# Kernel optimization log

Measured on AMD Instinct MI355X. Metric: run time of the kernel, lower is better.

Reference implementation:

```python
import jax, jax.numpy as jnp
import numpy as np

T, B, C, H, W = 40, 256, 32, 8, 8
D = C * H * W  # 2048 flattened enc dim


def setup_inputs() -> dict:
    key = jax.random.key(0)
    k0, k1, k2 = jax.random.split(key, 3)
    x = jax.random.normal(k0, (T, B, C, H, W), dtype=jnp.float32)
    W0 = jax.random.normal(k1, (4 * C, 2 * C, 5, 5), dtype=jnp.float32) * 0.05
    b0 = jnp.zeros((4 * C,), dtype=jnp.float32)
    W1 = jax.random.normal(k2, (4 * C, 2 * C, 3, 3), dtype=jnp.float32) * 0.05
    b1 = jnp.zeros((4 * C,), dtype=jnp.float32)
    return {"x": x, "W0": W0, "b0": b0, "W1": W1, "b1": b1}


def _conv(x, w, b, pad):
    y = jax.lax.conv_general_dilated(
        x, w, window_strides=(1, 1), padding=[(pad, pad), (pad, pad)],
        dimension_numbers=("NCHW", "OIHW", "NCHW"))
    return y + b[None, :, None, None]


def _cell(inp, h, c, w, b, pad):
    # ConvLSTMCell: conv over concat(input, hidden) -> 4 gates
    g = _conv(jnp.concatenate([inp, h], axis=1), w, b, pad)
    i_g, f_g, o_g, c_g = jnp.split(g, 4, axis=1)
    c_new = jax.nn.sigmoid(f_g) * c + jax.nn.sigmoid(i_g) * jnp.tanh(c_g)
    h_new = jax.nn.sigmoid(o_g) * jnp.tanh(c_new)
    return h_new, c_new


def reference(x, W0, b0, W1, b1):
    Tn, Bn, Cn, Hn, Wn = x.shape
    Dn = Cn * Hn * Wn
    zeros = jnp.zeros((Bn, Cn, Hn, Wn), x.dtype)
    buf0 = jnp.zeros((Tn, Bn, Dn), x.dtype)  # growing prev_encs buffer, masked
    steps = jnp.arange(Tn)

    def body(carry, xt_t):
        xt, t = xt_t
        h0, c0, h1, c1, buf = carry
        h0, c0 = _cell(xt, h0, c0, W0, b0, 2)  # cell0: k=5, pad=2
        flat = h0.reshape(Bn, Dn)
        buf = buf.at[t].set(flat)
        # attention over encs[0..t] (softmax over a single entry at t=0 -> enc itself)
        dots = jnp.einsum("bd,tbd->bt", flat, buf)
        dots = jnp.where((steps <= t)[None, :], dots, -jnp.inf)
        wts = jax.nn.softmax(dots, axis=1)
        att = jnp.einsum("bt,tbd->bd", wts, buf).reshape(Bn, Cn, Hn, Wn)
        h1, c1 = _cell(att, h1, c1, W1, b1, 1)  # cell1: k=3, pad=1
        return (h0, c0, h1, c1, buf), h1

    _, ys = jax.lax.scan(body, (zeros, zeros, zeros, zeros, buf0), (x, steps))
    return ys  # [T, B, C, 8, 8]
```

## Files before the change

### kernel.cpp

```cpp
#include <hip/hip_runtime.h>

#define TT 40
#define NB 256
#define DD 2048
#define HISTL 28

typedef __bf16 bf16x8 __attribute__((ext_vector_type(8)));
typedef float f32x4 __attribute__((ext_vector_type(4)));
typedef unsigned short u16;
typedef unsigned int u32;
typedef u16 u16x8 __attribute__((ext_vector_type(8)));
typedef u16 u16x4 __attribute__((ext_vector_type(4)));

__device__ __forceinline__ u16 f2bf(float f) {
  u32 u = __builtin_bit_cast(u32, f);
  return (u16)((u + 0x7fffu + ((u >> 16) & 1u)) >> 16);
}
__device__ __forceinline__ float bf2f(u16 h) {
  return __builtin_bit_cast(float, ((u32)h) << 16);
}
__device__ __forceinline__ bf16x8 asbf(u16x8 v) { return __builtin_bit_cast(bf16x8, v); }

__device__ __forceinline__ float sigm(float x) { return 1.0f / (1.0f + __expf(-x)); }
__device__ __forceinline__ float tanh_(float x) {
  float e = __expf(-2.0f * fabsf(x));
  float t = (1.0f - e) / (1.0f + e);
  return copysignf(t, x);
}

__device__ __forceinline__ f32x4 mfma16(bf16x8 a, bf16x8 b, f32x4 c) {
  return __builtin_amdgcn_mfma_f32_16x16x32_bf16(a, b, c, 0, 0, 0);
}

__device__ __forceinline__ int imin(int a, int b) { return a < b ? a : b; }

__global__ void prep_weights(const float* __restrict__ W0, const float* __restrict__ W1,
                             u16* __restrict__ A0, u16* __restrict__ A1) {
  int tid = blockIdx.x * 256 + threadIdx.x;
  if (tid < 25600) {
    int lane = tid & 63;
    int kt = tid >> 9;
    int p = ((tid >> 6) & 7) * 16 + (lane & 15);
    int oc = (p & 3) * 32 + ((p >> 5) & 3) * 8 + ((p >> 4) & 1) * 4 + ((p >> 2) & 3);
    int kb = kt * 32 + (lane >> 4) * 8;
#pragma unroll
    for (int j = 0; j < 8; ++j) {
      int k = kb + j;
      int pos = k >> 6, ic = k & 63;
      int ky = pos / 5, kx = pos - ky * 5;
      A0[tid * 8 + j] = f2bf(W0[((oc * 64 + ic) * 5 + ky) * 5 + kx]);
    }
  } else if (tid < 25600 + 9216) {
    int t2 = tid - 25600;
    int lane = t2 & 63;
    int kt = t2 >> 9;
    int p = ((t2 >> 6) & 7) * 16 + (lane & 15);
    int oc = (p & 3) * 32 + ((p >> 5) & 3) * 8 + ((p >> 4) & 1) * 4 + ((p >> 2) & 3);
    int kb = kt * 32 + (lane >> 4) * 8;
#pragma unroll
    for (int j = 0; j < 8; ++j) {
      int k = kb + j;
      int pos = k >> 6, ic = k & 63;
      int ky = pos / 3, kx = pos - ky * 3;
      A1[t2 * 8 + j] = f2bf(W1[((oc * 64 + ic) * 3 + ky) * 3 + kx]);
    }
  }
}

template <int KK, int NKT, int SKB, int DEPTH>
__device__ __forceinline__ void conv_loop2(const u16* __restrict__ wsA, const u16* img,
                                           int wg, int lane, f32x4 acc[2][4]) {
  const int ic0v = (lane >> 4) << 3;
  const int pb0 = ((lane & 15) >> 3) * 12 + (lane & 7);
  const bf16x8* A = (const bf16x8*)wsA;
  const int aidx = 2 * wg * 64 + lane;
  bf16x8 r0[DEPTH], r1[DEPTH];
#pragma unroll
  for (int i = 0; i < DEPTH; ++i) {
    r0[i] = A[aidx + i * 512];
    r1[i] = A[aidx + i * 512 + 64];
  }
#pragma unroll
  for (int kt = 0; kt < NKT; ++kt) {
    const int slot = kt % DEPTH;
    const bf16x8 c0 = r0[slot];
    const bf16x8 c1 = r1[slot];
    if (kt + DEPTH < NKT) {
      r0[slot] = A[aidx + (kt + DEPTH) * 512];
      r1[slot] = A[aidx + (kt + DEPTH) * 512 + 64];
    }
    const int pos = kt >> 1, ih = kt & 1;
    const int ky = pos / KK, kx = pos - ky * KK;
    const int Pb = pb0 + (ky * 12 + kx + SKB);
    const int idx = Pb * 64 + ((ic0v ^ ((Pb & 7) << 3)) ^ (ih << 5));
    u16x8 b0v = *(const u16x8*)(img + idx);
    u16x8 b1v = *(const u16x8*)(img + idx + 1536);
    u16x8 b2v = *(const u16x8*)(img + idx + 3072);
    u16x8 b3v = *(const u16x8*)(img + idx + 4608);
    acc[0][0] = mfma16(c0, asbf(b0v), acc[0][0]);
    acc[1][0] = mfma16(c1, asbf(b0v), acc[1][0]);
    acc[0][1] = mfma16(c0, asbf(b1v), acc[0][1]);
    acc[1][1] = mfma16(c1, asbf(b1v), acc[1][1]);
    acc[0][2] = mfma16(c0, asbf(b2v), acc[0][2]);
    acc[1][2] = mfma16(c1, asbf(b2v), acc[1][2]);
    acc[0][3] = mfma16(c0, asbf(b3v), acc[0][3]);
    acc[1][3] = mfma16(c1, asbf(b3v), acc[1][3]);
  }
}

__global__ void __launch_bounds__(512, 1)
convlstm_main(const float* __restrict__ x, const float* __restrict__ b0g,
              const float* __restrict__ b1g, const u16* __restrict__ wsA0,
              const u16* __restrict__ wsA1, u16* __restrict__ buf,
              float* __restrict__ out) {
  alignas(16) __shared__ u16 imgA[9216];
  alignas(16) __shared__ u16 imgB[9216];
  alignas(16) __shared__ u16 hist[HISTL * DD];
  alignas(16) __shared__ u16 curr[2 * DD];
  __shared__ float sdots[64];

  const int tid = threadIdx.x;
  const int b = blockIdx.x;
  const int lane = tid & 63;
  const int w = tid >> 6;
  const bool isA = (w < 4);
  const int wg = w & 3;
  const int h = lane >> 4;
  const int l15 = lane & 15;
  const int ch0 = 8 * wg + h;

  for (int i = tid; i < 9216; i += 512) {
    imgA[i] = 0;
    imgB[i] = 0;
  }

  float cst[2][4] = {};
  float bi[2][4];
  {
    const float* bg = isA ? b0g : b1g;
#pragma unroll
    for (int mi = 0; mi < 2; ++mi)
#pragma unroll
      for (int j = 0; j < 4; ++j) bi[mi][j] = bg[j * 32 + ch0 + 4 * mi];
  }

  const int Pldx = ((lane >> 3) + 2) * 12 + (lane & 7) + 2;
  const int swx = (Pldx & 7) << 3;
  const int Pl0 = ((l15 >> 3) + 2) * 12 + (l15 & 7) + 2;
  const int swh = (Pl0 & 7) << 3;
  const int bt = tid & 255;
  const int e8 = bt * 8;
  const int chB = bt >> 3;

  __syncthreads();

  float xr[8];
  if (isA) {
    const float* xp0 = x + (size_t)b * DD;
#pragma unroll
    for (int i = 0; i < 8; ++i) {
      int c = i * 4 + wg;
      imgA[Pldx * 64 + (c ^ swx)] = f2bf(xp0[c * 64 + lane]);
    }
    const float* xp1 = x + (size_t)(NB + b) * DD;
#pragma unroll
    for (int i = 0; i < 8; ++i) xr[i] = xp1[(i * 4 + wg) * 64 + lane];
  }

  __syncthreads();

  for (int s = 0; s <= TT + 1; ++s) {
    f32x4 acc[2][4];
    f32x4 zz = {0.f, 0.f, 0.f, 0.f};
#pragma unroll
    for (int mi = 0; mi < 2; ++mi)
#pragma unroll
      for (int nt = 0; nt < 4; ++nt) acc[mi][nt] = zz;

    if (isA) {
      if (s < TT) conv_loop2<5, 50, 0, 8>(wsA0, imgA, wg, lane, acc);
    } else {
      if (s >= 2) conv_loop2<3, 18, 13, 6>(wsA1, imgB, wg, lane, acc);
      const int t1 = s - 1;
      if (t1 >= 0 && t1 < TT) {
        u16x8 fv[4];
        const u16x8* rowT = (const u16x8*)&curr[(t1 & 1) * DD];
#pragma unroll
        for (int i = 0; i < 4; ++i) fv[i] = rowT[i * 64 + lane];
        int tp = wg;
        for (; tp <= t1 && tp < HISTL; tp += 4) {
          const u16x8* rowP = (const u16x8*)&hist[tp * DD];
          u16x8 p0 = rowP[lane], p1 = rowP[64 + lane], p2 = rowP[128 + lane],
                p3 = rowP[192 + lane];
          float d0 = 0.f, d1 = 0.f, d2 = 0.f, d3 = 0.f;
#pragma unroll
          for (int j = 0; j < 8; ++j) {
            d0 += bf2f(fv[0][j]) * bf2f(p0[j]);
            d1 += bf2f(fv[1][j]) * bf2f(p1[j]);
            d2 += bf2f(fv[2][j]) * bf2f(p2[j]);
            d3 += bf2f(fv[3][j]) * bf2f(p3[j]);
          }
          float dsum = (d0 + d1) + (d2 + d3);
#pragma unroll
          for (int off = 32; off; off >>= 1) dsum += __shfl_xor(dsum, off, 64);
          if (lane == 0) sdots[tp] = dsum;
        }
        for (; tp < t1; tp += 4) {
          const u16x8* rowP = (const u16x8*)(buf + (size_t)(tp * NB + b) * DD);
          u16x8 p0 = rowP[lane], p1 = rowP[64 + lane], p2 = rowP[128 + lane],
                p3 = rowP[192 + lane];
          float d0 = 0.f, d1 = 0.f, d2 = 0.f, d3 = 0.f;
#pragma unroll
          for (int j = 0; j < 8; ++j) {
            d0 += bf2f(fv[0][j]) * bf2f(p0[j]);
            d1 += bf2f(fv[1][j]) * bf2f(p1[j]);
            d2 += bf2f(fv[2][j]) * bf2f(p2[j]);
            d3 += bf2f(fv[3][j]) * bf2f(p3[j]);
          }
          float dsum = (d0 + d1) + (d2 + d3);
#pragma unroll
          for (int off = 32; off; off >>= 1) dsum += __shfl_xor(dsum, off, 64);
          if (lane == 0) sdots[tp] = dsum;
        }
        if (tp == t1) {
          float d0 = 0.f, d1 = 0.f, d2 = 0.f, d3 = 0.f;
#pragma unroll
          for (int j = 0; j < 8; ++j) {
            d0 += bf2f(fv[0][j]) * bf2f(fv[0][j]);
            d1 += bf2f(fv[1][j]) * bf2f(fv[1][j]);
            d2 += bf2f(fv[2][j]) * bf2f(fv[2][j]);
            d3 += bf2f(fv[3][j]) * bf2f(fv[3][j]);
          }
          float dsum = (d0 + d1) + (d2 + d3);
#pragma unroll
          for (int off = 32; off; off >>= 1) dsum += __shfl_xor(dsum, off, 64);
          if (lane == 0) sdots[tp] = dsum;
        }
      }
    }
    __syncthreads();

    if (isA) {
      if (s < TT) {
        u16* bufrow = buf + (size_t)(s * NB + b) * DD;
        u16* crow = &curr[(s & 1) * DD];
#pragma unroll
        for (int mi = 0; mi < 2; ++mi) {
          const int chm = ch0 + 4 * mi;
          u16x4 hv4;
#pragma unroll
          for (int nt = 0; nt < 4; ++nt) {
            float ig = acc[mi][nt][0] + bi[mi][0];
            float fg = acc[mi][nt][1] + bi[mi][1];
            float og = acc[mi][nt][2] + bi[mi][2];
            float cg = acc[mi][nt][3] + bi[mi][3];
            float cn = sigm(fg) * cst[mi][nt] + sigm(ig) * tanh_(cg);
            float hn = sigm(og) * tanh_(cn);
            cst[mi][nt] = cn;
            u16 hv = f2bf(hn);
            hv4[nt] = hv;
            imgA[(Pl0 + 24 * nt) * 64 + ((32 + chm) ^ swh)] = hv;
          }
          const int dbase = chm * 64 + l15 * 4;
          *(u16x4*)&crow[dbase] = hv4;
          if (s < HISTL)
            *(u16x4*)&hist[s * DD + dbase] = hv4;
          else
            *(u16x4*)(bufrow + dbase) = hv4;
        }
        if (s + 1 < TT) {
#pragma unroll
          for (int i = 0; i < 8; ++i) {
            int c = i * 4 + wg;
            imgA[Pldx * 64 + (c ^ swx)] = f2bf(xr[i]);
          }
        }
        if (s + 2 < TT) {
          const float* xp = x + (size_t)((s + 2) * NB + b) * DD;
#pragma unroll
          for (int i = 0; i < 8; ++i) xr[i] = xp[(i * 4 + wg) * 64 + lane];
        }
      }
    } else {
      const int t2 = s - 2;
      if (t2 >= 0) {
        float* outrow = out + (size_t)(t2 * NB + b) * DD;
#pragma unroll
        for (int mi = 0; mi < 2; ++mi) {
          const int chm = ch0 + 4 * mi;
#pragma unroll
          for (int nt = 0; nt < 4; ++nt) {
            float ig = acc[mi][nt][0] + bi[mi][0];
            float fg = acc[mi][nt][1] + bi[mi][1];
            float og = acc[mi][nt][2] + bi[mi][2];
            float cg = acc[mi][nt][3] + bi[mi][3];
            float cn = sigm(fg) * cst[mi][nt] + sigm(ig) * tanh_(cg);
            float hn = sigm(og) * tanh_(cn);
            cst[mi][nt] = cn;
            imgB[(Pl0 + 24 * nt) * 64 + ((32 + chm) ^ swh)] = f2bf(hn);
            outrow[chm * 64 + nt * 16 + l15] = hn;
          }
        }
      }
      const int t1 = s - 1;
      if (t1 >= 0 && t1 < TT) {
        float myw;
        {
          float v = (lane <= t1) ? sdots[lane] : -3.0e38f;
          float m = v;
#pragma unroll
          for (int off = 32; off; off >>= 1) m = fmaxf(m, __shfl_xor(m, off, 64));
          float e = (lane <= t1) ? __expf(v - m) : 0.f;
          float ss = e;
#pragma unroll
          for (int off = 32; off; off >>= 1) ss += __shfl_xor(ss, off, 64);
          myw = e / ss;
        }
        float av[8] = {0.f, 0.f, 0.f, 0.f, 0.f, 0.f, 0.f, 0.f};
        const int lim = imin(t1, HISTL);
        int tp = 0;
        for (; tp < lim; ++tp) {
          float wt = __shfl(myw, tp, 64);
          u16x8 v = *(const u16x8*)&hist[tp * DD + e8];
#pragma unroll
          for (int j = 0; j < 8; ++j) av[j] = fmaf(wt, bf2f(v[j]), av[j]);
        }
        for (tp = HISTL; tp < t1; ++tp) {
          float wt = __shfl(myw, tp, 64);
          u16x8 v = *(const u16x8*)(buf + (size_t)(tp * NB + b) * DD + e8);
#pragma unroll
          for (int j = 0; j < 8; ++j) av[j] = fmaf(wt, bf2f(v[j]), av[j]);
        }
        {
          float wt = __shfl(myw, t1, 64);
          u16x8 v = *(const u16x8*)&curr[(t1 & 1) * DD + e8];
#pragma unroll
          for (int j = 0; j < 8; ++j) av[j] = fmaf(wt, bf2f(v[j]), av[j]);
        }
#pragma unroll
        for (int j = 0; j < 8; ++j) {
          const int pixel = (j & 3) * 16 + (bt & 7) * 2 + (j >> 2);
          const int P = ((pixel >> 3) + 2) * 12 + (pixel & 7) + 2;
          imgB[P * 64 + (chB ^ ((P & 7) << 3))] = f2bf(av[j]);
        }
      }
    }
    __syncthreads();
  }
}

extern "C" void kernel_launch(void* const* d_in, const int* in_sizes, int n_in,
                              void* d_out, int out_size, void* d_ws, size_t ws_size,
                              hipStream_t stream) {
  const float* x = (const float*)d_in[0];
  const float* W0 = (const float*)d_in[1];
  const float* b0 = (const float*)d_in[2];
  const float* W1 = (const float*)d_in[3];
  const float* b1 = (const float*)d_in[4];
  float* out = (float*)d_out;

  u16* A0 = (u16*)d_ws;
  u16* A1 = A0 + 204800;
  u16* buf = (u16*)((char*)d_ws + (1 << 20));

  prep_weights<<<136, 256, 0, stream>>>(W0, W1, A0, A1);
  convlstm_main<<<256, 512, 0, stream>>>(x, b0, b1, A0, A1, buf, out);
}
```

Before: 1.313 ms.

## Double block size to 1024 threads, splitting conv M-tiles across twice the waves

Raises the workgroup from 8 to 16 waves so each wave computes one 16-row MFMA M-tile instead of two, and redistributes the attention dot products, weighted sum and x loading over the extra waves. It also swaps shuffle-based weight broadcast for readlane and unrolls the global-history loop by two. The aim is more latency hiding on this serial recurrent kernel with one block per CU. The cost is more waves per block synchronizing every step and fewer registers available per thread.

```diff
diff --git a/kernel.cpp b/kernel.cpp
--- a/kernel.cpp
+++ b/kernel.cpp
@@ -33,6 +33,10 @@
 }
 
 __device__ __forceinline__ int imin(int a, int b) { return a < b ? a : b; }
+
+__device__ __forceinline__ float rdlane(float v, int l) {
+  return __builtin_bit_cast(float, __builtin_amdgcn_readlane(__builtin_bit_cast(int, v), l));
+}
 
 __global__ void prep_weights(const float* __restrict__ W0, const float* __restrict__ W1,
                              u16* __restrict__ A0, u16* __restrict__ A1) {
@@ -68,27 +72,20 @@
 }
 
 template <int KK, int NKT, int SKB, int DEPTH>
-__device__ __forceinline__ void conv_loop2(const u16* __restrict__ wsA, const u16* img,
-                                           int wg, int lane, f32x4 acc[2][4]) {
+__device__ __forceinline__ void conv_loop1(const u16* __restrict__ wsA, const u16* img,
+                                           int wg, int lane, f32x4 acc[4]) {
   const int ic0v = (lane >> 4) << 3;
   const int pb0 = ((lane & 15) >> 3) * 12 + (lane & 7);
   const bf16x8* A = (const bf16x8*)wsA;
-  const int aidx = 2 * wg * 64 + lane;
-  bf16x8 r0[DEPTH], r1[DEPTH];
-#pragma unroll
-  for (int i = 0; i < DEPTH; ++i) {
-    r0[i] = A[aidx + i * 512];
-    r1[i] = A[aidx + i * 512 + 64];
-  }
+  const int aidx = wg * 64 + lane;
+  bf16x8 r[DEPTH];
+#pragma unroll
+  for (int i = 0; i < DEPTH; ++i) r[i] = A[aidx + i * 512];
 #pragma unroll
   for (int kt = 0; kt < NKT; ++kt) {
     const int slot = kt % DEPTH;
-    const bf16x8 c0 = r0[slot];
-    const bf16x8 c1 = r1[slot];
-    if (kt + DEPTH < NKT) {
-      r0[slot] = A[aidx + (kt + DEPTH) * 512];
-      r1[slot] = A[aidx + (kt + DEPTH) * 512 + 64];
-    }
+    const bf16x8 c0 = r[slot];
+    if (kt + DEPTH < NKT) r[slot] = A[aidx + (kt + DEPTH) * 512];
     const int pos = kt >> 1, ih = kt & 1;
     const int ky = pos / KK, kx = pos - ky * KK;
     const int Pb = pb0 + (ky * 12 + kx + SKB);
@@ -97,18 +94,14 @@
     u16x8 b1v = *(const u16x8*)(img + idx + 1536);
     u16x8 b2v = *(const u16x8*)(img + idx + 3072);
     u16x8 b3v = *(const u16x8*)(img + idx + 4608);
-    acc[0][0] = mfma16(c0, asbf(b0v), acc[0][0]);
-    acc[1][0] = mfma16(c1, asbf(b0v), acc[1][0]);
-    acc[0][1] = mfma16(c0, asbf(b1v), acc[0][1]);
-    acc[1][1] = mfma16(c1, asbf(b1v), acc[1][1]);
-    acc[0][2] = mfma16(c0, asbf(b2v), acc[0][2]);
-    acc[1][2] = mfma16(c1, asbf(b2v), acc[1][2]);
-    acc[0][3] = mfma16(c0, asbf(b3v), acc[0][3]);
-    acc[1][3] = mfma16(c1, asbf(b3v), acc[1][3]);
-  }
-}
-
-__global__ void __launch_bounds__(512, 1)
+    acc[0] = mfma16(c0, asbf(b0v), acc[0]);
+    acc[1] = mfma16(c0, asbf(b1v), acc[1]);
+    acc[2] = mfma16(c0, asbf(b2v), acc[2]);
+    acc[3] = mfma16(c0, asbf(b3v), acc[3]);
+  }
+}
+
+__global__ void __launch_bounds__(1024, 1)
 convlstm_main(const float* __restrict__ x, const float* __restrict__ b0g,
               const float* __restrict__ b1g, const u16* __restrict__ wsA0,
               const u16* __restrict__ wsA1, u16* __restrict__ buf,
@@ -123,64 +116,60 @@
   const int b = blockIdx.x;
   const int lane = tid & 63;
   const int w = tid >> 6;
-  const bool isA = (w < 4);
-  const int wg = w & 3;
+  const bool isA = (w < 8);
+  const int wg = w & 7;
   const int h = lane >> 4;
   const int l15 = lane & 15;
-  const int ch0 = 8 * wg + h;
-
-  for (int i = tid; i < 9216; i += 512) {
+  const int ch = ((wg >> 1) & 3) * 8 + (wg & 1) * 4 + h;
+
+  for (int i = tid; i < 9216; i += 1024) {
     imgA[i] = 0;
     imgB[i] = 0;
   }
 
-  float cst[2][4] = {};
-  float bi[2][4];
+  float cst[4] = {};
+  float bi[4];
   {
     const float* bg = isA ? b0g : b1g;
 #pragma unroll
-    for (int mi = 0; mi < 2; ++mi)
-#pragma unroll
-      for (int j = 0; j < 4; ++j) bi[mi][j] = bg[j * 32 + ch0 + 4 * mi];
+    for (int j = 0; j < 4; ++j) bi[j] = bg[j * 32 + ch];
   }
 
   const int Pldx = ((lane >> 3) + 2) * 12 + (lane & 7) + 2;
   const int swx = (Pldx & 7) << 3;
   const int Pl0 = ((l15 >> 3) + 2) * 12 + (l15 & 7) + 2;
   const int swh = (Pl0 & 7) << 3;
-  const int bt = tid & 255;
-  const int e8 = bt * 8;
-  const int chB = bt >> 3;
+  const int btB = tid & 511;
+  const int e4 = btB * 4;
+  const int chB = btB >> 4;
+  const int plB = btB & 15;
 
   __syncthreads();
 
-  float xr[8];
+  float xr[4];
   if (isA) {
     const float* xp0 = x + (size_t)b * DD;
-#pragma unroll
-    for (int i = 0; i < 8; ++i) {
-      int c = i * 4 + wg;
-      imgA[Pldx * 64 + (c ^ swx)] = f2bf(xp0[c * 64 + lane]);
-    }
+    u16x4 xv;
+#pragma unroll
+    for (int i = 0; i < 4; ++i) xv[i] = f2bf(xp0[(wg * 4 + i) * 64 + lane]);
+    *(u16x4*)&imgA[Pldx * 64 + ((wg * 4) ^ swx)] = xv;
     const float* xp1 = x + (size_t)(NB + b) * DD;
 #pragma unroll
-    for (int i = 0; i < 8; ++i) xr[i] = xp1[(i * 4 + wg) * 64 + lane];
+    for (int i = 0; i < 4; ++i) xr[i] = xp1[(wg * 4 + i) * 64 + lane];
   }
 
   __syncthreads();
 
   for (int s = 0; s <= TT + 1; ++s) {
-    f32x4 acc[2][4];
+    f32x4 acc[4];
     f32x4 zz = {0.f, 0.f, 0.f, 0.f};
 #pragma unroll
-    for (int mi = 0; mi < 2; ++mi)
-#pragma unroll
-      for (int nt = 0; nt < 4; ++nt) acc[mi][nt] = zz;
+    for (int nt = 0; nt < 4; ++nt) acc[nt] = zz;
 
     if (isA) {
-      if (s < TT) conv_loop2<5, 50, 0, 8>(wsA0, imgA, wg, lane, acc);
+      if (s < TT) conv_loop1<5, 50, 0, 8>(wsA0, imgA, wg, lane, acc);
     } else {
-      if (s >= 2) conv_loop2<3, 18, 13, 6>(wsA1, imgB, wg, lane, acc);
+      if (s >= 2) conv_loop1<3, 18, 13, 6>(wsA1, imgB, wg, lane, acc);
       const int t1 = s - 1;
       if (t1 >= 0 && t1 < TT) {
         u16x8 fv[4];
@@ -188,7 +177,7 @@
 #pragma unroll
         for (int i = 0; i < 4; ++i) fv[i] = rowT[i * 64 + lane];
         int tp = wg;
-        for (; tp <= t1 && tp < HISTL; tp += 4) {
+        for (; tp <= t1 && tp < HISTL; tp += 8) {
           const u16x8* rowP = (const u16x8*)&hist[tp * DD];
           u16x8 p0 = rowP[lane], p1 = rowP[64 + lane], p2 = rowP[128 + lane],
                 p3 = rowP[192 + lane];
@@ -205,7 +194,7 @@
           for (int off = 32; off; off >>= 1) dsum += __shfl_xor(dsum, off, 64);
           if (lane == 0) sdots[tp] = dsum;
         }
-        for (; tp < t1; tp += 4) {
+        for (; tp < t1; tp += 8) {
           const u16x8* rowP = (const u16x8*)(buf + (size_t)(tp * NB + b) * DD);
           u16x8 p0 = rowP[lane], p1 = rowP[64 + lane], p2 = rowP[128 + lane],
                 p3 = rowP[192 + lane];
@@ -222,7 +211,7 @@
           for (int off = 32; off; off >>= 1) dsum += __shfl_xor(dsum, off, 64);
           if (lane == 0) sdots[tp] = dsum;
         }
-        if (tp == t1) {
+        if (t1 >= HISTL && (t1 & 7) == wg) {
           float d0 = 0.f, d1 = 0.f, d2 = 0.f, d3 = 0.f;
 #pragma unroll
           for (int j = 0; j < 8; ++j) {
@@ -234,7 +223,7 @@
           float dsum = (d0 + d1) + (d2 + d3);
 #pragma unroll
           for (int off = 32; off; off >>= 1) dsum += __shfl_xor(dsum, off, 64);
-          if (lane == 0) sdots[tp] = dsum;
+          if (lane == 0) sdots[t1] = dsum;
         }
       }
     }
@@ -244,41 +233,36 @@
       if (s < TT) {
         u16* bufrow = buf + (size_t)(s * NB + b) * DD;
         u16* crow = &curr[(s & 1) * DD];
-#pragma unroll
-        for (int mi = 0; mi < 2; ++mi) {
-          const int chm = ch0 + 4 * mi;
-          u16x4 hv4;
-#pragma unroll
-          for (int nt = 0; nt < 4; ++nt) {
-            float ig = acc[mi][nt][0] + bi[mi][0];
-            float fg = acc[mi][nt][1] + bi[mi][1];
-            float og = acc[mi][nt][2] + bi[mi][2];
-            float cg = acc[mi][nt][3] + bi[mi][3];
-            float cn = sigm(fg) * cst[mi][nt] + sigm(ig) * tanh_(cg);
-            float hn = sigm(og) * tanh_(cn);
-            cst[mi][nt] = cn;
-            u16 hv = f2bf(hn);
-            hv4[nt] = hv;
-            imgA[(Pl0 + 24 * nt) * 64 + ((32 + chm) ^ swh)] = hv;
-          }
-          const int dbase = chm * 64 + l15 * 4;
-          *(u16x4*)&crow[dbase] = hv4;
-          if (s < HISTL)
-            *(u16x4*)&hist[s * DD + dbase] = hv4;
-          else
-            *(u16x4*)(bufrow + dbase) = hv4;
-        }
+        u16x4 hv4;
+#pragma unroll
+        for (int nt = 0; nt < 4; ++nt) {
+          float ig = acc[nt][0] + bi[0];
+          float fg = acc[nt][1] + bi[1];
+          float og = acc[nt][2] + bi[2];
+          float cg = acc[nt][3] + bi[3];
+          float cn = sigm(fg) * cst[nt] + sigm(ig) * tanh_(cg);
+          float hn = sigm(og) * tanh_(cn);
+          cst[nt] = cn;
+          u16 hv = f2bf(hn);
+          hv4[nt] = hv;
+          imgA[(Pl0 + 24 * nt) * 64 + ((32 + ch) ^ swh)] = hv;
+        }
+        const int dbase = ch * 64 + l15 * 4;
+        *(u16x4*)&crow[dbase] = hv4;
+        if (s < HISTL)
+          *(u16x4*)&hist[s * DD + dbase] = hv4;
+        else
+          *(u16x4*)(bufrow + dbase) = hv4;
         if (s + 1 < TT) {
-#pragma unroll
-          for (int i = 0; i < 8; ++i) {
-            int c = i * 4 + wg;
-            imgA[Pldx * 64 + (c ^ swx)] = f2bf(xr[i]);
-          }
+          u16x4 xv;
+#pragma unroll
+          for (int i = 0; i < 4; ++i) xv[i] = f2bf(xr[i]);
+          *(u16x4*)&imgA[Pldx * 64 + ((wg * 4) ^ swx)] = xv;
         }
         if (s + 2 < TT) {
           const float* xp = x + (size_t)((s + 2) * NB + b) * DD;
 #pragma unroll
-          for (int i = 0; i < 8; ++i) xr[i] = xp[(i * 4 + wg) * 64 + lane];
+          for (int i = 0; i < 4; ++i) xr[i] = xp[(wg * 4 + i) * 64 + lane];
         }
       }
     } else {
@@ -286,20 +270,16 @@
       if (t2 >= 0) {
         float* outrow = out + (size_t)(t2 * NB + b) * DD;
 #pragma unroll
-        for (int mi = 0; mi < 2; ++mi) {
-          const int chm = ch0 + 4 * mi;
-#pragma unroll
-          for (int nt = 0; nt < 4; ++nt) {
-            float ig = acc[mi][nt][0] + bi[mi][0];
-            float fg = acc[mi][nt][1] + bi[mi][1];
-            float og = acc[mi][nt][2] + bi[mi][2];
-            float cg = acc[mi][nt][3] + bi[mi][3];
-            float cn = sigm(fg) * cst[mi][nt] + sigm(ig) * tanh_(cg);
-            float hn = sigm(og) * tanh_(cn);
-            cst[mi][nt] = cn;
-            imgB[(Pl0 + 24 * nt) * 64 + ((32 + chm) ^ swh)] = f2bf(hn);
-            outrow[chm * 64 + nt * 16 + l15] = hn;
-          }
+        for (int nt = 0; nt < 4; ++nt) {
+          float ig = acc[nt][0] + bi[0];
+          float fg = acc[nt][1] + bi[1];
+          float og = acc[nt][2] + bi[2];
+          float cg = acc[nt][3] + bi[3];
+          float cn = sigm(fg) * cst[nt] + sigm(ig) * tanh_(cg);
+          float hn = sigm(og) * tanh_(cn);
+          cst[nt] = cn;
+          imgB[(Pl0 + 24 * nt) * 64 + ((32 + ch) ^ swh)] = f2bf(hn);
+          outrow[ch * 64 + nt * 16 + l15] = hn;
         }
       }
       const int t1 = s - 1;
@@ -316,30 +296,52 @@
           for (int off = 32; off; off >>= 1) ss += __shfl_xor(ss, off, 64);
           myw = e / ss;
         }
-        float av[8] = {0.f, 0.f, 0.f, 0.f, 0.f, 0.f, 0.f, 0.f};
+        float av0 = 0.f, av1 = 0.f, av2 = 0.f, av3 = 0.f;
         const int lim = imin(t1, HISTL);
-        int tp = 0;
-        for (; tp < lim; ++tp) {
-          float wt = __shfl(myw, tp, 64);
-          u16x8 v = *(const u16x8*)&hist[tp * DD + e8];
-#pragma unroll
-          for (int j = 0; j < 8; ++j) av[j] = fmaf(wt, bf2f(v[j]), av[j]);
-        }
-        for (tp = HISTL; tp < t1; ++tp) {
-          float wt = __shfl(myw, tp, 64);
-          u16x8 v = *(const u16x8*)(buf + (size_t)(tp * NB + b) * DD + e8);
-#pragma unroll
-          for (int j = 0; j < 8; ++j) av[j] = fmaf(wt, bf2f(v[j]), av[j]);
+        for (int tp = 0; tp < lim; ++tp) {
+          float wt = rdlane(myw, tp);
+          u16x4 v = *(const u16x4*)&hist[tp * DD + e4];
+          av0 = fmaf(wt, bf2f(v[0]), av0);
+          av1 = fmaf(wt, bf2f(v[1]), av1);
+          av2 = fmaf(wt, bf2f(v[2]), av2);
+          av3 = fmaf(wt, bf2f(v[3]), av3);
         }
         {
-          float wt = __shfl(myw, t1, 64);
-          u16x8 v = *(const u16x8*)&curr[(t1 & 1) * DD + e8];
-#pragma unroll
-          for (int j = 0; j < 8; ++j) av[j] = fmaf(wt, bf2f(v[j]), av[j]);
-        }
-#pragma unroll
-        for (int j = 0; j < 8; ++j) {
-          const int pixel = (j & 3) * 16 + (bt & 7) * 2 + (j >> 2);
+          int tp = HISTL;
+          for (; tp + 1 < t1; tp += 2) {
+            float wa = rdlane(myw, tp), wb = rdlane(myw, tp + 1);
+            u16x4 va = *(const u16x4*)(buf + (size_t)(tp * NB + b) * DD + e4);
+            u16x4 vb = *(const u16x4*)(buf + (size_t)((tp + 1) * NB + b) * DD + e4);
+            av0 = fmaf(wa, bf2f(va[0]), av0);
+            av1 = fmaf(wa, bf2f(va[1]), av1);
+            av2 = fmaf(wa, bf2f(va[2]), av2);
+            av3 = fmaf(wa, bf2f(va[3]), av3);
+            av0 = fmaf(wb, bf2f(vb[0]), av0);
+            av1 = fmaf(wb, bf2f(vb[1]), av1);
+            av2 = fmaf(wb, bf2f(vb[2]), av2);
+            av3 = fmaf(wb, bf2f(vb[3]), av3);
+          }
+          if (tp < t1) {
+            float wa = rdlane(myw, tp);
+            u16x4 va = *(const u16x4*)(buf + (size_t)(tp * NB + b) * DD + e4);
+            av0 = fmaf(wa, bf2f(va[0]), av0);
+            av1 = fmaf(wa, bf2f(va[1]), av1);
+            av2 = fmaf(wa, bf2f(va[2]), av2);
+            av3 = fmaf(wa, bf2f(va[3]), av3);
+          }
+        }
+        {
+          float wt = rdlane(myw, t1);
+          u16x4 v = *(const u16x4*)&curr[(t1 & 1) * DD + e4];
+          av0 = fmaf(wt, bf2f(v[0]), av0);
+          av1 = fmaf(wt, bf2f(v[1]), av1);
+          av2 = fmaf(wt, bf2f(v[2]), av2);
+          av3 = fmaf(wt, bf2f(v[3]), av3);
+        }
+        float av[4] = {av0, av1, av2, av3};
+#pragma unroll
+        for (int j = 0; j < 4; ++j) {
+          const int pixel = j * 16 + plB;
           const int P = ((pixel >> 3) + 2) * 12 + (pixel & 7) + 2;
           imgB[P * 64 + (chB ^ ((P & 7) << 3))] = f2bf(av[j]);
         }
@@ -364,5 +366,5 @@
   u16* buf = (u16*)((char*)d_ws + (1 << 20));
 
   prep_weights<<<136, 256, 0, stream>>>(W0, W1, A0, A1);
-  convlstm_main<<<256, 512, 0, stream>>>(x, b0, b1, A0, A1, buf, out);
-}
+  convlstm_main<<<256, 1024, 0, stream>>>(x, b0, b1, A0, A1, buf, out);
+}
```

Result: slower. 1.545 ms (+17.7%).

## Split attention weighted-sum across all warps and vectorize input image staging

Applied to the files above, without the earlier changes.

The attention weighted sum moves out of the B-group-only branch so all 512 threads share it, each handling 4 elements instead of 8. It uses readlane scalar broadcasts in place of shuffles and unrolls the history loop by two. Input staging now packs 8 consecutive channels into one 16-byte LDS store instead of 8 scalar stores. The sdots index fix (tp to t1) is equivalent because tp==t1 in that branch. Giving the A-group warps this extra work could lengthen their critical path, and the output pixel mapping changes.

```diff
diff --git a/kernel.cpp b/kernel.cpp
--- a/kernel.cpp
+++ b/kernel.cpp
@@ -33,6 +33,10 @@
 }
 
 __device__ __forceinline__ int imin(int a, int b) { return a < b ? a : b; }
+
+__device__ __forceinline__ float rdlane(float v, int l) {
+  return __builtin_bit_cast(float, __builtin_amdgcn_readlane(__builtin_bit_cast(int, v), l));
+}
 
 __global__ void prep_weights(const float* __restrict__ W0, const float* __restrict__ W1,
                              u16* __restrict__ A0, u16* __restrict__ A1) {
@@ -148,23 +152,22 @@
   const int swx = (Pldx & 7) << 3;
   const int Pl0 = ((l15 >> 3) + 2) * 12 + (l15 & 7) + 2;
   const int swh = (Pl0 & 7) << 3;
-  const int bt = tid & 255;
-  const int e8 = bt * 8;
-  const int chB = bt >> 3;
+  const int e4 = tid * 4;
+  const int chAtt = tid >> 4;
+  const int plA = tid & 15;
 
   __syncthreads();
 
   float xr[8];
   if (isA) {
     const float* xp0 = x + (size_t)b * DD;
-#pragma unroll
-    for (int i = 0; i < 8; ++i) {
-      int c = i * 4 + wg;
-      imgA[Pldx * 64 + (c ^ swx)] = f2bf(xp0[c * 64 + lane]);
-    }
+    u16x8 xv;
+#pragma unroll
+    for (int i = 0; i < 8; ++i) xv[i] = f2bf(xp0[(wg * 8 + i) * 64 + lane]);
+    *(u16x8*)&imgA[Pldx * 64 + ((wg * 8) ^ swx)] = xv;
     const float* xp1 = x + (size_t)(NB + b) * DD;
 #pragma unroll
-    for (int i = 0; i < 8; ++i) xr[i] = xp1[(i * 4 + wg) * 64 + lane];
+    for (int i = 0; i < 8; ++i) xr[i] = xp1[(wg * 8 + i) * 64 + lane];
   }
 
   __syncthreads();
@@ -234,7 +237,7 @@
           float dsum = (d0 + d1) + (d2 + d3);
 #pragma unroll
           for (int off = 32; off; off >>= 1) dsum += __shfl_xor(dsum, off, 64);
-          if (lane == 0) sdots[tp] = dsum;
+          if (lane == 0) sdots[t1] = dsum;
         }
       }
     }
@@ -269,16 +272,15 @@
             *(u16x4*)(bufrow + dbase) = hv4;
         }
         if (s + 1 < TT) {
-#pragma unroll
-          for (int i = 0; i < 8; ++i) {
-            int c = i * 4 + wg;
-            imgA[Pldx * 64 + (c ^ swx)] = f2bf(xr[i]);
-          }
+          u16x8 xv;
+#pragma unroll
+          for (int i = 0; i < 8; ++i) xv[i] = f2bf(xr[i]);
+          *(u16x8*)&imgA[Pldx * 64 + ((wg * 8) ^ swx)] = xv;
         }
         if (s + 2 < TT) {
           const float* xp = x + (size_t)((s + 2) * NB + b) * DD;
 #pragma unroll
-          for (int i = 0; i < 8; ++i) xr[i] = xp[(i * 4 + wg) * 64 + lane];
+          for (int i = 0; i < 8; ++i) xr[i] = xp[(wg * 8 + i) * 64 + lane];
         }
       }
     } else {
@@ -302,6 +304,8 @@
           }
         }
       }
+    }
+    {
       const int t1 = s - 1;
       if (t1 >= 0 && t1 < TT) {
         float myw;
@@ -316,32 +320,66 @@
           for (int off = 32; off; off >>= 1) ss += __shfl_xor(ss, off, 64);
           myw = e / ss;
         }
-        float av[8] = {0.f, 0.f, 0.f, 0.f, 0.f, 0.f, 0.f, 0.f};
+        float av0 = 0.f, av1 = 0.f, av2 = 0.f, av3 = 0.f;
         const int lim = imin(t1, HISTL);
         int tp = 0;
-        for (; tp < lim; ++tp) {
-          float wt = __shfl(myw, tp, 64);
-          u16x8 v = *(const u16x8*)&hist[tp * DD + e8];
-#pragma unroll
-          for (int j = 0; j < 8; ++j) av[j] = fmaf(wt, bf2f(v[j]), av[j]);
-        }
-        for (tp = HISTL; tp < t1; ++tp) {
-          float wt = __shfl(myw, tp, 64);
-          u16x8 v = *(const u16x8*)(buf + (size_t)(tp * NB + b) * DD + e8);
-#pragma unroll
-          for (int j = 0; j < 8; ++j) av[j] = fmaf(wt, bf2f(v[j]), av[j]);
+        for (; tp + 1 < lim; tp += 2) {
+          float wa = rdlane(myw, tp), wb = rdlane(myw, tp + 1);
+          u16x4 va = *(const u16x4*)&hist[tp * DD + e4];
+          u16x4 vb = *(const u16x4*)&hist[(tp + 1) * DD + e4];
+          av0 = fmaf(wa, bf2f(va[0]), av0);
+          av1 = fmaf(wa, bf2f(va[1]), av1);
+          av2 = fmaf(wa, bf2f(va[2]), av2);
+          av3 = fmaf(wa, bf2f(va[3]), av3);
+          av0 = fmaf(wb, bf2f(vb[0]), av0);
+          av1 = fmaf(wb, bf2f(vb[1]), av1);
+          av2 = fmaf(wb, bf2f(vb[2]), av2);
+          av3 = fmaf(wb, bf2f(vb[3]), av3);
+        }
+        if (tp < lim) {
+          float wa = rdlane(myw, tp);
+          u16x4 va = *(const u16x4*)&hist[tp * DD + e4];
+          av0 = fmaf(wa, bf2f(va[0]), av0);
+          av1 = fmaf(wa, bf2f(va[1]), av1);
+          av2 = fmaf(wa, bf2f(va[2]), av2);
+          av3 = fmaf(wa, bf2f(va[3]), av3);
+        }
+        tp = HISTL;
+        for (; tp + 1 < t1; tp += 2) {
+          float wa = rdlane(myw, tp), wb = rdlane(myw, tp + 1);
+          u16x4 va = *(const u16x4*)(buf + (size_t)(tp * NB + b) * DD + e4);
+          u16x4 vb = *(const u16x4*)(buf + (size_t)((tp + 1) * NB + b) * DD + e4);
+          av0 = fmaf(wa, bf2f(va[0]), av0);
+          av1 = fmaf(wa, bf2f(va[1]), av1);
+          av2 = fmaf(wa, bf2f(va[2]), av2);
+          av3 = fmaf(wa, bf2f(va[3]), av3);
+          av0 = fmaf(wb, bf2f(vb[0]), av0);
+          av1 = fmaf(wb, bf2f(vb[1]), av1);
+          av2 = fmaf(wb, bf2f(vb[2]), av2);
+          av3 = fmaf(wb, bf2f(vb[3]), av3);
+        }
+        if (tp < t1) {
+          float wa = rdlane(myw, tp);
+          u16x4 va = *(const u16x4*)(buf + (size_t)(tp * NB + b) * DD + e4);
+          av0 = fmaf(wa, bf2f(va[0]), av0);
+          av1 = fmaf(wa, bf2f(va[1]), av1);
+          av2 = fmaf(wa, bf2f(va[2]), av2);
+          av3 = fmaf(wa, bf2f(va[3]), av3);
         }
         {
-          float wt = __shfl(myw, t1, 64);
-          u16x8 v = *(const u16x8*)&curr[(t1 & 1) * DD + e8];
-#pragma unroll
-          for (int j = 0; j < 8; ++j) av[j] = fmaf(wt, bf2f(v[j]), av[j]);
-        }
-#pragma unroll
-        for (int j = 0; j < 8; ++j) {
-          const int pixel = (j & 3) * 16 + (bt & 7) * 2 + (j >> 2);
+          float wt = rdlane(myw, t1);
+          u16x4 v = *(const u16x4*)&curr[(t1 & 1) * DD + e4];
+          av0 = fmaf(wt, bf2f(v[0]), av0);
+          av1 = fmaf(wt, bf2f(v[1]), av1);
+          av2 = fmaf(wt, bf2f(v[2]), av2);
+          av3 = fmaf(wt, bf2f(v[3]), av3);
+        }
+        float av[4] = {av0, av1, av2, av3};
+#pragma unroll
+        for (int j = 0; j < 4; ++j) {
+          const int pixel = j * 16 + plA;
           const int P = ((pixel >> 3) + 2) * 12 + (pixel & 7) + 2;
-          imgB[P * 64 + (chB ^ ((P & 7) << 3))] = f2bf(av[j]);
+          imgB[P * 64 + (chAtt ^ ((P & 7) << 3))] = f2bf(av[j]);
         }
       }
     }
```

Result: no change. 1.295 ms, median of 2 (-1.4%).
